# Performance work log

Measured on AMD Instinct MI355X. Metric: run time of the kernel, lower is better.

## Reference

```python
import jax, jax.numpy as jnp
import numpy as np

EPS = 1e-5  # torch InstanceNorm2d default eps


def setup_inputs() -> dict:
    key = jax.random.key(0)
    k1, k2, k3, k4, k5 = jax.random.split(key, 5)
    # shapes forced by the module: h*w == 64 (Linear(64,192)), (n,s,c) == (25,128,2)
    inp = jax.random.normal(k1, (25, 2, 128, 8, 8), dtype=jnp.float32)
    qkv_w = jax.random.normal(k2, (192, 64), dtype=jnp.float32) * 0.125
    qkv_b = jax.random.normal(k3, (192,), dtype=jnp.float32) * 0.02
    proj_w = jax.random.normal(k4, (64, 64), dtype=jnp.float32) * 0.125
    proj_b = jax.random.normal(k5, (64,), dtype=jnp.float32) * 0.02
    return {"inp": inp, "qkv_w": qkv_w, "qkv_b": qkv_b,
            "proj_w": proj_w, "proj_b": proj_b}


def reference(inp, qkv_w, qkv_b, proj_w, proj_b):
    n, c, s, h, w = inp.shape  # (25, 2, 128, 8, 8)
    hw = h * w  # 64
    # view(n,c,s,hw).transpose(1,2) -> (n, s, c, hw)
    x = jnp.transpose(inp.reshape(n, c, s, hw), (0, 2, 1, 3))
    # InstanceNorm2d(affine=False): normalize over the last two dims (c, hw)
    # per (n, s) instance, biased variance, eps=1e-5.
    mean = jnp.mean(x, axis=(2, 3), keepdims=True)
    var = jnp.var(x, axis=(2, 3), keepdims=True)
    x = (x - mean) * jax.lax.rsqrt(var + EPS)
    # fused QKV projection on the hw(=64) dim
    qkv = x @ qkv_w.T + qkv_b  # (n, s, c, 192)
    q, k, v = jnp.split(qkv, 3, axis=-1)  # each (n, s, c, 64)
    # linear attention: out = v + q @ (k^T @ v); the 'lower' branch in the
    # original is dead code (never used), so it is omitted.
    kv = jnp.einsum('nscd,nsce->nsde', k, v)  # (n, s, 64, 64)
    attn = v + jnp.einsum('nscd,nsde->nsce', q, kv)  # (n, s, c, 64)
    out = attn @ proj_w.T + proj_b  # dropout is identity in eval mode
    # transpose(1,2).reshape(n,c,s,h,w), residual, final merge of (c,s)
    out = jnp.transpose(out, (0, 2, 1, 3)).reshape(n, c, s, h, w)
    return (out + inp).reshape(n, c * s, h, w)
```

## Files before the change

### kernel.cpp

```cpp
#include <hip/hip_runtime.h>

#define EPS 1e-5f


typedef _Float16 half8 __attribute__((ext_vector_type(8)));
typedef float    f32x4 __attribute__((ext_vector_type(4)));

__device__ __forceinline__ half8 cvt8(float4 a, float4 b) {
    half8 h;
    h[0] = (_Float16)a.x; h[1] = (_Float16)a.y; h[2] = (_Float16)a.z; h[3] = (_Float16)a.w;
    h[4] = (_Float16)b.x; h[5] = (_Float16)b.y; h[6] = (_Float16)b.z; h[7] = (_Float16)b.w;
    return h;
}

__device__ __forceinline__ int swz(int row, int colByte) {
    return row * 128 + (colByte ^ ((row & 7) << 4));
}

__global__ __launch_bounds__(64)
void attn_mfma(const float* __restrict__ inp,
               const float* __restrict__ qkv_w,
               const float* __restrict__ qkv_b,
               const float* __restrict__ proj_w,
               const float* __restrict__ proj_b,
               float* __restrict__ out)
{
    __shared__ _Float16 a_lds[16 * 64];

    const int l  = threadIdx.x;
    const int lr = l & 15;
    const int lg = l >> 4;

    const int R = blockIdx.x * 16 + lr;
    const int g = R >> 1, c = R & 1;
    const int n = g >> 7, s = g & 127;
    const int rowbase = n * 16384 + c * 8192 + s * 64;
    const int col0 = lg * 8;

    const float4 x0a = *reinterpret_cast<const float4*>(inp + rowbase + col0);
    const float4 x0b = *reinterpret_cast<const float4*>(inp + rowbase + col0 + 4);
    const float4 x1a = *reinterpret_cast<const float4*>(inp + rowbase + col0 + 32);
    const float4 x1b = *reinterpret_cast<const float4*>(inp + rowbase + col0 + 36);

    half8 pw0[4], pw1[4];
    #pragma unroll
    for (int nt = 0; nt < 4; ++nt) {
        const float* pb = proj_w + (nt * 16 + lr) * 64 + lg * 8;
        pw0[nt] = cvt8(*reinterpret_cast<const float4*>(pb),
                       *reinterpret_cast<const float4*>(pb + 4));
        pw1[nt] = cvt8(*reinterpret_cast<const float4*>(pb + 32),
                       *reinterpret_cast<const float4*>(pb + 36));
    }

    float s1 = (x0a.x + x0a.y) + (x0a.z + x0a.w) + (x0b.x + x0b.y) + (x0b.z + x0b.w)
             + (x1a.x + x1a.y) + (x1a.z + x1a.w) + (x1b.x + x1b.y) + (x1b.z + x1b.w);
    float s2 = x0a.x*x0a.x + x0a.y*x0a.y + x0a.z*x0a.z + x0a.w*x0a.w
             + x0b.x*x0b.x + x0b.y*x0b.y + x0b.z*x0b.z + x0b.w*x0b.w
             + x1a.x*x1a.x + x1a.y*x1a.y + x1a.z*x1a.z + x1a.w*x1a.w
             + x1b.x*x1b.x + x1b.y*x1b.y + x1b.z*x1b.z + x1b.w*x1b.w;
    s1 += __shfl_xor(s1, 1);  s2 += __shfl_xor(s2, 1);
    s1 += __shfl_xor(s1, 16); s2 += __shfl_xor(s2, 16);
    s1 += __shfl_xor(s1, 32); s2 += __shfl_xor(s2, 32);
    const float mean = s1 * (1.0f / 128.0f);
    const float var  = s2 * (1.0f / 128.0f) - mean * mean;
    const float rs   = rsqrtf(var + EPS);

    half8 a0, a1;
    a0[0]=(_Float16)((x0a.x-mean)*rs); a0[1]=(_Float16)((x0a.y-mean)*rs);
    a0[2]=(_Float16)((x0a.z-mean)*rs); a0[3]=(_Float16)((x0a.w-mean)*rs);
    a0[4]=(_Float16)((x0b.x-mean)*rs); a0[5]=(_Float16)((x0b.y-mean)*rs);
    a0[6]=(_Float16)((x0b.z-mean)*rs); a0[7]=(_Float16)((x0b.w-mean)*rs);
    a1[0]=(_Float16)((x1a.x-mean)*rs); a1[1]=(_Float16)((x1a.y-mean)*rs);
    a1[2]=(_Float16)((x1a.z-mean)*rs); a1[3]=(_Float16)((x1a.w-mean)*rs);
    a1[4]=(_Float16)((x1b.x-mean)*rs); a1[5]=(_Float16)((x1b.y-mean)*rs);
    a1[6]=(_Float16)((x1b.z-mean)*rs); a1[7]=(_Float16)((x1b.w-mean)*rs);

    f32x4 acc[12];
    #pragma unroll
    for (int nt = 0; nt < 12; ++nt) acc[nt] = f32x4{0.f, 0.f, 0.f, 0.f};
    #pragma unroll
    for (int nt = 0; nt < 12; ++nt) {
        const float* wb = qkv_w + (nt * 16 + lr) * 64 + lg * 8;
        const half8 b0 = cvt8(*reinterpret_cast<const float4*>(wb),
                              *reinterpret_cast<const float4*>(wb + 4));
        const half8 b1 = cvt8(*reinterpret_cast<const float4*>(wb + 32),
                              *reinterpret_cast<const float4*>(wb + 36));
        acc[nt] = __builtin_amdgcn_mfma_f32_16x16x32_f16(a0, b0, acc[nt], 0, 0, 0);
        acc[nt] = __builtin_amdgcn_mfma_f32_16x16x32_f16(a1, b1, acc[nt], 0, 0, 0);
    }
    #pragma unroll
    for (int nt = 0; nt < 12; ++nt) {
        const float b = qkv_b[nt * 16 + lr];
        acc[nt].x += b; acc[nt].y += b; acc[nt].z += b; acc[nt].w += b;
    }

    float p[8] = {0.f,0.f,0.f,0.f,0.f,0.f,0.f,0.f};
    #pragma unroll
    for (int nt = 0; nt < 4; ++nt) {
        const f32x4 q = acc[nt], k = acc[4 + nt];
        p[0] = fmaf(q.x, k.x, p[0]);  p[1] = fmaf(q.x, k.y, p[1]);
        p[2] = fmaf(q.y, k.x, p[2]);  p[3] = fmaf(q.y, k.y, p[3]);
        p[4] = fmaf(q.z, k.z, p[4]);  p[5] = fmaf(q.z, k.w, p[5]);
        p[6] = fmaf(q.w, k.z, p[6]);  p[7] = fmaf(q.w, k.w, p[7]);
    }
    #pragma unroll
    for (int m = 8; m >= 1; m >>= 1) {
        #pragma unroll
        for (int z = 0; z < 8; ++z) p[z] += __shfl_xor(p[z], m);
    }
    #pragma unroll
    for (int nt = 0; nt < 4; ++nt) {
        const f32x4 v = acc[8 + nt];
        float av[4];
        av[0] = v.x + fmaf(p[0], v.x, p[1] * v.y);
        av[1] = v.y + fmaf(p[2], v.x, p[3] * v.y);
        av[2] = v.z + fmaf(p[4], v.z, p[5] * v.w);
        av[3] = v.w + fmaf(p[6], v.z, p[7] * v.w);
        #pragma unroll
        for (int r = 0; r < 4; ++r) {
            const int row  = lg * 4 + r;
            const int colB = (nt * 16 + lr) * 2;
            *reinterpret_cast<_Float16*>(
                reinterpret_cast<char*>(a_lds) + swz(row, colB)) = (_Float16)av[r];
        }
    }
    __syncthreads();

    const half8 a20 = *reinterpret_cast<const half8*>(
        reinterpret_cast<const char*>(a_lds) + swz(lr, lg * 16));
    const half8 a21 = *reinterpret_cast<const half8*>(
        reinterpret_cast<const char*>(a_lds) + swz(lr, lg * 16 + 64));
    f32x4 acc2[4];
    #pragma unroll
    for (int nt = 0; nt < 4; ++nt) acc2[nt] = f32x4{0.f, 0.f, 0.f, 0.f};
    #pragma unroll
    for (int nt = 0; nt < 4; ++nt) {
        acc2[nt] = __builtin_amdgcn_mfma_f32_16x16x32_f16(a20, pw0[nt], acc2[nt], 0, 0, 0);
        acc2[nt] = __builtin_amdgcn_mfma_f32_16x16x32_f16(a21, pw1[nt], acc2[nt], 0, 0, 0);
    }

    #pragma unroll
    for (int nt = 0; nt < 4; ++nt) {
        const int col = nt * 16 + lr;
        const float pb = proj_b[col];
        #pragma unroll
        for (int r = 0; r < 4; ++r) {
            const int Rg = blockIdx.x * 16 + lg * 4 + r;
            const int gi = Rg >> 1, cc = Rg & 1;
            const int nn = gi >> 7, ss = gi & 127;
            const int addr = nn * 16384 + cc * 8192 + ss * 64 + col;
            const float a = (r == 0) ? acc2[nt].x : (r == 1) ? acc2[nt].y
                          : (r == 2) ? acc2[nt].z : acc2[nt].w;
            out[addr] = a + pb + inp[addr];
        }
    }
}

extern "C" void kernel_launch(void* const* d_in, const int* in_sizes, int n_in,
                              void* d_out, int out_size, void* d_ws, size_t ws_size,
                              hipStream_t stream) {
    const float* inp    = (const float*)d_in[0];
    const float* qkv_w  = (const float*)d_in[1];
    const float* qkv_b  = (const float*)d_in[2];
    const float* proj_w = (const float*)d_in[3];
    const float* proj_b = (const float*)d_in[4];
    float* out = (float*)d_out;

    attn_mfma<<<dim3(400), dim3(64), 0, stream>>>(inp, qkv_w, qkv_b, proj_w, proj_b, out);
}
```

Baseline: 12.18 us.

## Stage QKV weights in LDS shared by two waves per block

Each block now runs two waves over 32 rows and launches half as many blocks. The block cooperatively converts the full 192x64 QKV weight to fp16 once into swizzled LDS, and both waves read their MFMA B operands from there. Before, every wave loaded and converted its own copy straight from global memory. The bias loads are also hoisted ahead of the compute. In exchange there is an extra block barrier and 24KB of LDS per block, and only 200 blocks run, which may underfill the GPU's CUs.

Measured after the change: 9.985 us. 18.0% less time.

```diff
diff --git a/kernel.cpp b/kernel.cpp
--- a/kernel.cpp
+++ b/kernel.cpp
@@ -17,7 +17,7 @@
     return row * 128 + (colByte ^ ((row & 7) << 4));
 }
 
-__global__ __launch_bounds__(64)
+__global__ __launch_bounds__(128)
 void attn_mfma(const float* __restrict__ inp,
                const float* __restrict__ qkv_w,
                const float* __restrict__ qkv_b,
@@ -25,13 +25,17 @@
                const float* __restrict__ proj_b,
                float* __restrict__ out)
 {
-    __shared__ _Float16 a_lds[16 * 64];
+    __shared__ __align__(16) _Float16 w_lds[192 * 64];
+    __shared__ __align__(16) _Float16 a_lds[32 * 64];
 
-    const int l  = threadIdx.x;
-    const int lr = l & 15;
-    const int lg = l >> 4;
+    const int tid = threadIdx.x;
+    const int w   = tid >> 6;
+    const int l   = tid & 63;
+    const int lr  = l & 15;
+    const int lg  = l >> 4;
 
-    const int R = blockIdx.x * 16 + lr;
+    const int lrow = (w << 4) | lr;
+    const int R = blockIdx.x * 32 + lrow;
     const int g = R >> 1, c = R & 1;
     const int n = g >> 7, s = g & 127;
     const int rowbase = n * 16384 + c * 8192 + s * 64;
@@ -42,6 +46,17 @@
     const float4 x1a = *reinterpret_cast<const float4*>(inp + rowbase + col0 + 32);
     const float4 x1b = *reinterpret_cast<const float4*>(inp + rowbase + col0 + 36);
 
+    #pragma unroll
+    for (int k = 0; k < 12; ++k) {
+        const int idx8 = tid + k * 128;
+        const float4 f0 = reinterpret_cast<const float4*>(qkv_w)[idx8 * 2];
+        const float4 f1 = reinterpret_cast<const float4*>(qkv_w)[idx8 * 2 + 1];
+        const int row  = idx8 >> 3;
+        const int colB = (idx8 & 7) * 16;
+        *reinterpret_cast<half8*>(reinterpret_cast<char*>(w_lds) + swz(row, colB)) =
+            cvt8(f0, f1);
+    }
+
     half8 pw0[4], pw1[4];
     #pragma unroll
     for (int nt = 0; nt < 4; ++nt) {
@@ -51,6 +66,12 @@
         pw1[nt] = cvt8(*reinterpret_cast<const float4*>(pb + 32),
                        *reinterpret_cast<const float4*>(pb + 36));
     }
+
+    float bq[12], pbv[4];
+    #pragma unroll
+    for (int nt = 0; nt < 12; ++nt) bq[nt] = qkv_b[nt * 16 + lr];
+    #pragma unroll
+    for (int nt = 0; nt < 4; ++nt)  pbv[nt] = proj_b[nt * 16 + lr];
 
     float s1 = (x0a.x + x0a.y) + (x0a.z + x0a.w) + (x0b.x + x0b.y) + (x0b.z + x0b.w)
              + (x1a.x + x1a.y) + (x1a.z + x1a.w) + (x1b.x + x1b.y) + (x1b.z + x1b.w);
@@ -75,23 +96,24 @@
     a1[4]=(_Float16)((x1b.x-mean)*rs); a1[5]=(_Float16)((x1b.y-mean)*rs);
     a1[6]=(_Float16)((x1b.z-mean)*rs); a1[7]=(_Float16)((x1b.w-mean)*rs);
 
+    __syncthreads();
+
     f32x4 acc[12];
     #pragma unroll
     for (int nt = 0; nt < 12; ++nt) acc[nt] = f32x4{0.f, 0.f, 0.f, 0.f};
     #pragma unroll
     for (int nt = 0; nt < 12; ++nt) {
-        const float* wb = qkv_w + (nt * 16 + lr) * 64 + lg * 8;
-        const half8 b0 = cvt8(*reinterpret_cast<const float4*>(wb),
-                              *reinterpret_cast<const float4*>(wb + 4));
-        const half8 b1 = cvt8(*reinterpret_cast<const float4*>(wb + 32),
-                              *reinterpret_cast<const float4*>(wb + 36));
+        const int o = nt * 16 + lr;
+        const half8 b0 = *reinterpret_cast<const half8*>(
+            reinterpret_cast<const char*>(w_lds) + swz(o, lg * 16));
+        const half8 b1 = *reinterpret_cast<const half8*>(
+            reinterpret_cast<const char*>(w_lds) + swz(o, lg * 16 + 64));
         acc[nt] = __builtin_amdgcn_mfma_f32_16x16x32_f16(a0, b0, acc[nt], 0, 0, 0);
         acc[nt] = __builtin_amdgcn_mfma_f32_16x16x32_f16(a1, b1, acc[nt], 0, 0, 0);
     }
     #pragma unroll
     for (int nt = 0; nt < 12; ++nt) {
-        const float b = qkv_b[nt * 16 + lr];
-        acc[nt].x += b; acc[nt].y += b; acc[nt].z += b; acc[nt].w += b;
+        acc[nt].x += bq[nt]; acc[nt].y += bq[nt]; acc[nt].z += bq[nt]; acc[nt].w += bq[nt];
     }
 
     float p[8] = {0.f,0.f,0.f,0.f,0.f,0.f,0.f,0.f};
@@ -118,7 +140,7 @@
         av[3] = v.w + fmaf(p[6], v.z, p[7] * v.w);
         #pragma unroll
         for (int r = 0; r < 4; ++r) {
-            const int row  = lg * 4 + r;
+            const int row  = (w << 4) + lg * 4 + r;
             const int colB = (nt * 16 + lr) * 2;
             *reinterpret_cast<_Float16*>(
                 reinterpret_cast<char*>(a_lds) + swz(row, colB)) = (_Float16)av[r];
@@ -127,9 +149,9 @@
     __syncthreads();
 
     const half8 a20 = *reinterpret_cast<const half8*>(
-        reinterpret_cast<const char*>(a_lds) + swz(lr, lg * 16));
+        reinterpret_cast<const char*>(a_lds) + swz(lrow, lg * 16));
     const half8 a21 = *reinterpret_cast<const half8*>(
-        reinterpret_cast<const char*>(a_lds) + swz(lr, lg * 16 + 64));
+        reinterpret_cast<const char*>(a_lds) + swz(lrow, lg * 16 + 64));
     f32x4 acc2[4];
     #pragma unroll
     for (int nt = 0; nt < 4; ++nt) acc2[nt] = f32x4{0.f, 0.f, 0.f, 0.f};
@@ -142,16 +164,15 @@
     #pragma unroll
     for (int nt = 0; nt < 4; ++nt) {
         const int col = nt * 16 + lr;
-        const float pb = proj_b[col];
         #pragma unroll
         for (int r = 0; r < 4; ++r) {
-            const int Rg = blockIdx.x * 16 + lg * 4 + r;
+            const int Rg = blockIdx.x * 32 + (w << 4) + lg * 4 + r;
             const int gi = Rg >> 1, cc = Rg & 1;
             const int nn = gi >> 7, ss = gi & 127;
             const int addr = nn * 16384 + cc * 8192 + ss * 64 + col;
             const float a = (r == 0) ? acc2[nt].x : (r == 1) ? acc2[nt].y
                           : (r == 2) ? acc2[nt].z : acc2[nt].w;
-            out[addr] = a + pb + inp[addr];
+            out[addr] = a + pbv[nt] + inp[addr];
         }
     }
 }
@@ -166,5 +187,5 @@
     const float* proj_b = (const float*)d_in[4];
     float* out = (float*)d_out;
 
-    attn_mfma<<<dim3(400), dim3(64), 0, stream>>>(inp, qkv_w, qkv_b, proj_w, proj_b, out);
+    attn_mfma<<<dim3(200), dim3(128), 0, stream>>>(inp, qkv_w, qkv_b, proj_w, proj_b, out);
 }
```
